# Kernel tuning notes

Measured on AMD Instinct MI355X. Metric: run time of the kernel, lower is better.

Reference implementation:

```python
import jax, jax.numpy as jnp
import numpy as np

N_NODES = 50000
N_EDGES = 1600000
GL = [512, 256, 16]
LL = [16, 16]


def setup_inputs() -> dict:
    key = jax.random.key(0)
    ks = jax.random.split(key, 10)
    H = jax.random.normal(ks[0], (N_NODES, GL[0]), dtype=jnp.float32)
    edge_index = jax.random.randint(ks[1], (2, N_EDGES), 0, N_NODES, dtype=jnp.int64)
    edge_vals = jax.random.uniform(ks[2], (N_EDGES,), dtype=jnp.float32)
    def uni(k, shape, fan_out):
        stdv = 1.0 / np.sqrt(fan_out)
        return jax.random.uniform(k, shape, minval=-stdv, maxval=stdv, dtype=jnp.float32)
    W1 = uni(ks[3], (GL[0], GL[1]), GL[1])
    b1 = uni(ks[4], (GL[1],), GL[1])
    W2 = uni(ks[5], (GL[1], GL[2]), GL[2])
    b2 = uni(ks[6], (GL[2],), GL[2])
    Wl = uni(ks[7], (LL[0], LL[1]), LL[0])
    bl = uni(ks[8], (LL[1],), LL[0])
    return {"H": H, "edge_index": edge_index, "edge_vals": edge_vals,
            "W1": W1, "b1": b1, "W2": W2, "b2": b2, "Wl": Wl, "bl": bl}


def reference(H, edge_index, edge_vals, W1, b1, W2, b2, Wl, bl):
    row, col = edge_index[0], edge_index[1]
    n = H.shape[0]

    def spmm(X):  # (A @ X) for sparse COO A, X: [N, d]
        return jax.ops.segment_sum(edge_vals[:, None] * X[col], row, num_segments=n)

    # graph conv layers (dropout condition idx < len-2 never fires with 2 layers)
    H1 = jax.nn.relu(spmm(H @ W1) + b1)
    H2 = jax.nn.relu(spmm(H1 @ W2) + b2)
    # linear head
    H3 = jax.nn.relu(H2 @ Wl + bl)
    Y = jax.nn.softmax(H3, axis=1)  # [N, g]

    # NCut loss: sum_e w_e * dot(Y[row_e]/Gamma, (1-Y)[col_e])
    D = jax.ops.segment_sum(edge_vals, row, num_segments=n)  # degree [N]
    Gamma = Y.T @ D  # [g]
    YbyG = Y / Gamma[None, :]
    loss = jnp.sum(jnp.sum(YbyG[row] * (1.0 - Y)[col], axis=1) * edge_vals)
    return jnp.reshape(loss, (1,))
```

## Files before the change

### kernel.cpp

```cpp
#include <hip/hip_runtime.h>


constexpr int NN = 50000;
constexpr int NE = 1600000;
constexpr int F0 = 512;
constexpr int F1 = 256;
constexpr int G  = 16;
constexpr int CB   = 196;
constexpr int CCAP = 10240;
constexpr int CHUNK = 4096;
constexpr int NGEMM = 391 * 2;
constexpr int NPASS = 391;

typedef short  s16x8 __attribute__((ext_vector_type(8)));
typedef float  f32x4 __attribute__((ext_vector_type(4)));
typedef float  f32x2 __attribute__((ext_vector_type(2)));
typedef int    i32x4 __attribute__((ext_vector_type(4)));
typedef int    i32x2 __attribute__((ext_vector_type(2)));
typedef float  fv4   __attribute__((ext_vector_type(4)));

static __device__ __forceinline__ unsigned short f2bf(float f) {
    union { float f; unsigned u; } v; v.f = f;
    unsigned r = (v.u + 0x7FFFu + ((v.u >> 16) & 1u)) >> 16;
    return (unsigned short)r;
}
static __device__ __forceinline__ float bf2f(unsigned short u) {
    union { unsigned u; float f; } v; v.u = (unsigned)u << 16;
    return v.f;
}

__global__ __launch_bounds__(256) void k_castW1(const float* __restrict__ W1, unsigned short* __restrict__ W1t) {
    int idx = blockIdx.x * 256 + threadIdx.x;
    if (idx < F0 * F1) {
        int k = idx >> 8, n = idx & 255;
        W1t[n * F0 + k] = f2bf(W1[idx]);
    }
}

__global__ __launch_bounds__(256) void k_fused1(const float* __restrict__ H,
                                                const unsigned short* __restrict__ W1t,
                                                unsigned char* __restrict__ XW,
                                                const int* __restrict__ row, const int* __restrict__ col,
                                                const float* __restrict__ ev,
                                                int* __restrict__ ccur, int2* __restrict__ cbuf) {
    __shared__ __align__(16) unsigned char smem[2 * 128 * 72 * 2];
    const int bid = blockIdx.x;
    const int tid = threadIdx.x;
    const int stripe = bid / 3;
    const int pos = bid - stripe * 3;

    if (pos != 1) {
        const int gidx = stripe * 2 + (pos >> 1);
        unsigned short (*As)[72] = (unsigned short(*)[72])smem;
        unsigned short (*Bs)[72] = (unsigned short(*)[72])(smem + 128 * 72 * 2);
        const int lane = tid & 63;
        const int wave = tid >> 6;
        const int bm = (gidx >> 1) * 128;
        const int bn = (gidx & 1) * 128;
        const int m_off = (wave & 1) * 64;
        const int n_off = (wave >> 1) * 64;
        const int l15  = lane & 15;
        const int quad = lane >> 4;

        f32x4 acc[4][4];
#pragma unroll
        for (int i = 0; i < 4; ++i)
#pragma unroll
            for (int j = 0; j < 4; ++j) acc[i][j] = (f32x4)0.f;

        const int arow = tid >> 4;
        const int akq  = tid & 15;
        const int brow = tid >> 3;
        const int bkq  = tid & 7;

        float4 ar[8];
        uint4  br[4];

#define LOAD_TILE(K0)                                                              \
        do {                                                                       \
            _Pragma("unroll")                                                      \
            for (int p = 0; p < 8; ++p) {                                          \
                int gr = bm + p * 16 + arow;                                       \
                ar[p] = (gr < NN)                                                  \
                    ? *(const float4*)&H[(size_t)gr * F0 + (K0) + akq * 4]         \
                    : make_float4(0.f, 0.f, 0.f, 0.f);                             \
            }                                                                      \
            _Pragma("unroll")                                                      \
            for (int p = 0; p < 4; ++p)                                            \
                br[p] = *(const uint4*)&W1t[(size_t)(bn + p * 32 + brow) * F0 + (K0) + bkq * 8]; \
        } while (0)

        LOAD_TILE(0);
        for (int k0 = 0; k0 < F0; k0 += 64) {
#pragma unroll
            for (int p = 0; p < 8; ++p) {
                unsigned d0 = (unsigned)f2bf(ar[p].x) | ((unsigned)f2bf(ar[p].y) << 16);
                unsigned d1 = (unsigned)f2bf(ar[p].z) | ((unsigned)f2bf(ar[p].w) << 16);
                *(uint2*)&As[p * 16 + arow][akq * 4] = make_uint2(d0, d1);
            }
#pragma unroll
            for (int p = 0; p < 4; ++p)
                *(uint4*)&Bs[p * 32 + brow][bkq * 8] = br[p];
            __syncthreads();
            if (k0 + 64 < F0) LOAD_TILE(k0 + 64);
#pragma unroll
            for (int kk = 0; kk < 64; kk += 32) {
                s16x8 af[4], bfr[4];
#pragma unroll
                for (int mi = 0; mi < 4; ++mi)
                    af[mi] = *(const s16x8*)&As[m_off + mi * 16 + l15][kk + quad * 8];
#pragma unroll
                for (int ni = 0; ni < 4; ++ni)
                    bfr[ni] = *(const s16x8*)&Bs[n_off + ni * 16 + l15][kk + quad * 8];
#pragma unroll
                for (int mi = 0; mi < 4; ++mi)
#pragma unroll
                    for (int ni = 0; ni < 4; ++ni)
                        acc[mi][ni] = __builtin_amdgcn_mfma_f32_16x16x32_bf16(af[mi], bfr[ni], acc[mi][ni], 0, 0, 0);
            }
            __syncthreads();
        }
#undef LOAD_TILE
#pragma unroll
        for (int mi = 0; mi < 4; ++mi) {
            int r0 = bm + m_off + mi * 16 + quad * 4;
#pragma unroll
            for (int reg = 0; reg < 4; ++reg) {
                int gr = r0 + reg;
                if (gr < NN) {
                    unsigned char* orow = &XW[(size_t)gr * F1 + bn + n_off];
#pragma unroll
                    for (int ni = 0; ni < 4; ++ni) {
                        int pk = __builtin_amdgcn_cvt_pk_fp8_f32(acc[mi][ni][reg], 0.f, 0, false);
                        orow[ni * 16 + l15] = (unsigned char)(pk & 0xff);
                    }
                }
            }
        }
    } else {
        int* hcnt  = (int*)smem;
        int* hbase = hcnt + CB;
        for (int i = tid; i < CB; i += 256) hcnt[i] = 0;
        __syncthreads();

        const int base4 = stripe * (CHUNK / 4);
        int recx[16]; float recw[16]; int cb[16];
#pragma unroll
        for (int k = 0; k < 4; ++k) {
            int i4 = base4 + k * 256 + tid;
            bool ok = i4 < NE / 4;
            i32x4 r = ok ? __builtin_nontemporal_load(&((const i32x4*)row)[i4]) : (i32x4)0;
            i32x4 c = ok ? __builtin_nontemporal_load(&((const i32x4*)col)[i4]) : (i32x4)0;
            fv4   w = ok ? __builtin_nontemporal_load(&((const fv4*)ev)[i4])   : (fv4)0.f;
            int rr[4] = {r.x, r.y, r.z, r.w};
            int cc[4] = {c.x, c.y, c.z, c.w};
            float ww[4] = {w.x, w.y, w.z, w.w};
#pragma unroll
            for (int j = 0; j < 4; ++j) {
                int slot = k * 4 + j;
                if (ok) {
                    cb[slot] = rr[j] >> 8;
                    atomicAdd(&hcnt[cb[slot]], 1);
                } else {
                    cb[slot] = -1;
                }
                recx[slot] = (cc[j] << 16) | (rr[j] & 255);
                recw[slot] = ww[j];
            }
        }
        __syncthreads();
        for (int i = tid; i < CB; i += 256) {
            int cnt = hcnt[i];
            hbase[i] = (cnt > 0) ? atomicAdd(&ccur[i], cnt) : 0;
            hcnt[i] = 0;
        }
        __syncthreads();
#pragma unroll
        for (int slot = 0; slot < 16; ++slot) {
            if (cb[slot] >= 0) {
                int p = hbase[cb[slot]] + atomicAdd(&hcnt[cb[slot]], 1);
                cbuf[(size_t)cb[slot] * CCAP + p] = make_int2(recx[slot], __float_as_int(recw[slot]));
            }
        }
    }
}

__global__ __launch_bounds__(256) void k_passB(const int2* __restrict__ cbuf, const int* __restrict__ ccur,
                                               int* __restrict__ rowptr, int2* __restrict__ E) {
    __shared__ int cnt[256];
    __shared__ int scn[256];
    __shared__ int red[4];
    const int cbk = blockIdx.x;
    const int tid = threadIdx.x;
    cnt[tid] = 0;

    int b = 0;
    for (int i = tid; i < cbk; i += 256) b += ccur[i];
#pragma unroll
    for (int off = 1; off < 64; off <<= 1) b += __shfl_xor(b, off, 64);
    if ((tid & 63) == 0) red[tid >> 6] = b;
    __syncthreads();
    const int base = red[0] + red[1] + red[2] + red[3];

    const int total = ccur[cbk];
    const int2* src = cbuf + (size_t)cbk * CCAP;
    for (int i = tid; i < total; i += 256) atomicAdd(&cnt[src[i].x & 255], 1);
    __syncthreads();

    scn[tid] = cnt[tid];
    __syncthreads();
    for (int off = 1; off < 256; off <<= 1) {
        int t = (tid >= off) ? scn[tid - off] : 0;
        __syncthreads();
        scn[tid] += t;
        __syncthreads();
    }
    const int excl = scn[tid] - cnt[tid];
    const int r = (cbk << 8) + tid;
    if (r <= NN) rowptr[r] = base + excl;
    __syncthreads();
    cnt[tid] = base + excl;
    __syncthreads();
    for (int i = tid; i < total; i += 256) {
        int2 rec = src[i];
        int rl = rec.x & 255;
        int c  = (int)((unsigned)rec.x >> 16);
        int p = atomicAdd(&cnt[rl], 1);
        E[p] = make_int2(c << 8, rec.y);
    }
}

__global__ __launch_bounds__(256) void k_spmm1(const unsigned char* __restrict__ XW, const int* __restrict__ rowptr,
                                               const int2* __restrict__ E,
                                               const float* __restrict__ b1, const float* __restrict__ W2,
                                               unsigned short* __restrict__ Z, float* __restrict__ Dv) {
    __shared__ float W2T[G * F1];
    const int tid = threadIdx.x;
#pragma unroll
    for (int it = 0; it < 16; ++it)
        W2T[it * 256 + tid] = W2[tid * 16 + it];
    __syncthreads();
    const int lane16 = tid & 15;
    const int loff = lane16 * 16;
    const int n = blockIdx.x * 16 + (tid >> 4);
    const int s = rowptr[n];
    const int e = rowptr[n + 1];
    const i32x2* Ev = (const i32x2*)E;

    float acc[16];
#pragma unroll
    for (int q = 0; q < 16; ++q) acc[q] = 0.f;
    float wsum = 0.f;

    for (int i = s; i < e; i += 4) {
        int of[4]; float w[4];
#pragma unroll
        for (int k = 0; k < 4; ++k) {
            int idx = i + k;
            bool ok = idx < e;
            i32x2 ed = __builtin_nontemporal_load(&Ev[ok ? idx : s]);
            of[k] = ed.x; w[k] = ok ? __int_as_float(ed.y) : 0.f;
        }
        uint4 gg[4];
#pragma unroll
        for (int k = 0; k < 4; ++k)
            gg[k] = *(const uint4*)(XW + of[k] + loff);
#pragma unroll
        for (int k = 0; k < 4; ++k) {
            const unsigned gw[4] = {gg[k].x, gg[k].y, gg[k].z, gg[k].w};
#pragma unroll
            for (int q = 0; q < 4; ++q) {
                f32x2 lo = __builtin_amdgcn_cvt_pk_f32_fp8(gw[q], false);
                f32x2 hi = __builtin_amdgcn_cvt_pk_f32_fp8(gw[q], true);
                acc[q * 4 + 0] = fmaf(w[k], lo.x, acc[q * 4 + 0]);
                acc[q * 4 + 1] = fmaf(w[k], lo.y, acc[q * 4 + 1]);
                acc[q * 4 + 2] = fmaf(w[k], hi.x, acc[q * 4 + 2]);
                acc[q * 4 + 3] = fmaf(w[k], hi.y, acc[q * 4 + 3]);
            }
            wsum += w[k];
        }
    }
    if (lane16 == 0) Dv[n] = wsum;

#pragma unroll
    for (int q = 0; q < 4; ++q) {
        float4 bb = *(const float4*)&b1[loff + q * 4];
        acc[q * 4 + 0] = fmaxf(acc[q * 4 + 0] + bb.x, 0.f);
        acc[q * 4 + 1] = fmaxf(acc[q * 4 + 1] + bb.y, 0.f);
        acc[q * 4 + 2] = fmaxf(acc[q * 4 + 2] + bb.z, 0.f);
        acc[q * 4 + 3] = fmaxf(acc[q * 4 + 3] + bb.w, 0.f);
    }

    float p[G];
#pragma unroll
    for (int j = 0; j < G; ++j) {
        float pj = 0.f;
#pragma unroll
        for (int q = 0; q < 4; ++q) {
            float4 w4 = *(const float4*)&W2T[j * F1 + loff + q * 4];
            pj += acc[q * 4 + 0] * w4.x + acc[q * 4 + 1] * w4.y
                + acc[q * 4 + 2] * w4.z + acc[q * 4 + 3] * w4.w;
        }
        p[j] = pj;
    }
#pragma unroll
    for (int off = 1; off < 16; off <<= 1) {
#pragma unroll
        for (int j = 0; j < G; ++j) p[j] += __shfl_xor(p[j], off, 64);
    }
    if (lane16 == 0) {
        unsigned zp[8];
#pragma unroll
        for (int j = 0; j < 8; ++j)
            zp[j] = (unsigned)f2bf(p[2 * j]) | ((unsigned)f2bf(p[2 * j + 1]) << 16);
        uint4* zo = (uint4*)&Z[n * G];
        zo[0] = make_uint4(zp[0], zp[1], zp[2], zp[3]);
        zo[1] = make_uint4(zp[4], zp[5], zp[6], zp[7]);
    }
}

__global__ __launch_bounds__(256) void k_head(const unsigned short* __restrict__ Zb, const int* __restrict__ rowptr,
                                              const int2* __restrict__ E,
                                              const float* __restrict__ b2, const float* __restrict__ Wl,
                                              const float* __restrict__ bl, const float* __restrict__ Dv,
                                              unsigned short* __restrict__ Yb, float* __restrict__ GammaP) {
    __shared__ float WlS[G * G];
    __shared__ float gsh[G];
    const int tid = threadIdx.x;
    if (tid < G * G) WlS[tid] = Wl[tid];
    if (tid < G) gsh[tid] = 0.f;
    __syncthreads();
    const int lane = tid & 63;
    const int g = lane >> 3;
    const int d = lane & 7;
    const int n = blockIdx.x * 4 + (tid >> 6);
    const int s = __builtin_amdgcn_readfirstlane(rowptr[n]);
    const int e = __builtin_amdgcn_readfirstlane(rowptr[n + 1]);
    const char* Zc = (const char*)Zb;
    const i32x2* Ev = (const i32x2*)E;

    float a0 = 0.f, a1 = 0.f;
    for (int base = s; base < e; base += 16) {
        int i0 = base + g;
        int i1 = base + 8 + g;
        i32x2 e0 = __builtin_nontemporal_load(&Ev[(i0 < e) ? i0 : s]);
        i32x2 e1 = __builtin_nontemporal_load(&Ev[(i1 < e) ? i1 : s]);
        float w0 = (i0 < e) ? __int_as_float(e0.y) : 0.f;
        float w1 = (i1 < e) ? __int_as_float(e1.y) : 0.f;
        unsigned z0 = *(const unsigned*)(Zc + (e0.x >> 3) + d * 4);
        unsigned z1 = *(const unsigned*)(Zc + (e1.x >> 3) + d * 4);
        a0 = fmaf(w0, bf2f((unsigned short)(z0 & 0xffff)), a0);
        a1 = fmaf(w0, bf2f((unsigned short)(z0 >> 16)), a1);
        a0 = fmaf(w1, bf2f((unsigned short)(z1 & 0xffff)), a0);
        a1 = fmaf(w1, bf2f((unsigned short)(z1 >> 16)), a1);
    }
    a0 += __shfl_xor(a0, 8, 64);  a1 += __shfl_xor(a1, 8, 64);
    a0 += __shfl_xor(a0, 16, 64); a1 += __shfl_xor(a1, 16, 64);
    a0 += __shfl_xor(a0, 32, 64); a1 += __shfl_xor(a1, 32, 64);

    const int j = lane & 15;
    float e0v = __shfl(a0, j >> 1, 64);
    float e1v = __shfl(a1, j >> 1, 64);
    float accj = (j & 1) ? e1v : e0v;

    float h2 = fmaxf(accj + b2[j], 0.f);
    float s3 = 0.f;
#pragma unroll
    for (int k = 0; k < G; ++k) s3 = fmaf(__shfl(h2, k, 64), WlS[k * G + j], s3);
    float h3 = fmaxf(s3 + bl[j], 0.f);
    float m = h3;
    m = fmaxf(m, __shfl_xor(m, 1, 64));
    m = fmaxf(m, __shfl_xor(m, 2, 64));
    m = fmaxf(m, __shfl_xor(m, 4, 64));
    m = fmaxf(m, __shfl_xor(m, 8, 64));
    float ex = __expf(h3 - m);
    float se = ex;
    se += __shfl_xor(se, 1, 64);
    se += __shfl_xor(se, 2, 64);
    se += __shfl_xor(se, 4, 64);
    se += __shfl_xor(se, 8, 64);
    float y = ex / se;
    if (lane < G) {
        Yb[n * G + j] = f2bf(y);
        atomicAdd(&gsh[j], y * Dv[n]);
    }
    __syncthreads();
    if (tid < G) atomicAdd(&GammaP[(blockIdx.x & 63) * G + tid], gsh[tid]);
}

__global__ __launch_bounds__(256) void k_loss(const unsigned short* __restrict__ Yb, const int* __restrict__ rowptr,
                                              const int2* __restrict__ E, float* __restrict__ SjP) {
    __shared__ float sjsh[G];
    const int tid = threadIdx.x;
    if (tid < G) sjsh[tid] = 0.f;
    __syncthreads();
    const int lane = tid & 63;
    const int g = lane >> 3;
    const int d = lane & 7;
    const int n = blockIdx.x * 4 + (tid >> 6);
    const int s = __builtin_amdgcn_readfirstlane(rowptr[n]);
    const int e = __builtin_amdgcn_readfirstlane(rowptr[n + 1]);
    const char* Yc = (const char*)Yb;
    const i32x2* Ev = (const i32x2*)E;

    unsigned yr = *(const unsigned*)(Yc + ((size_t)n << 5) + d * 4);
    float y0 = bf2f((unsigned short)(yr & 0xffff));
    float y1 = bf2f((unsigned short)(yr >> 16));

    float s0 = 0.f, s1 = 0.f;
    for (int base = s; base < e; base += 16) {
        int i0 = base + g;
        int i1 = base + 8 + g;
        i32x2 e0 = __builtin_nontemporal_load(&Ev[(i0 < e) ? i0 : s]);
        i32x2 e1 = __builtin_nontemporal_load(&Ev[(i1 < e) ? i1 : s]);
        float w0 = (i0 < e) ? __int_as_float(e0.y) : 0.f;
        float w1 = (i1 < e) ? __int_as_float(e1.y) : 0.f;
        unsigned z0 = *(const unsigned*)(Yc + (e0.x >> 3) + d * 4);
        unsigned z1 = *(const unsigned*)(Yc + (e1.x >> 3) + d * 4);
        s0 = fmaf(w0 * y0, bf2f((unsigned short)(z0 & 0xffff)), s0);
        s1 = fmaf(w0 * y1, bf2f((unsigned short)(z0 >> 16)), s1);
        s0 = fmaf(w1 * y0, bf2f((unsigned short)(z1 & 0xffff)), s0);
        s1 = fmaf(w1 * y1, bf2f((unsigned short)(z1 >> 16)), s1);
    }
    s0 += __shfl_xor(s0, 8, 64);  s1 += __shfl_xor(s1, 8, 64);
    s0 += __shfl_xor(s0, 16, 64); s1 += __shfl_xor(s1, 16, 64);
    s0 += __shfl_xor(s0, 32, 64); s1 += __shfl_xor(s1, 32, 64);
    if (lane < 8) {
        atomicAdd(&sjsh[2 * lane],     s0);
        atomicAdd(&sjsh[2 * lane + 1], s1);
    }
    __syncthreads();
    if (tid < G) atomicAdd(&SjP[(blockIdx.x & 63) * G + tid], sjsh[tid]);
}

__global__ void k_final(const float* __restrict__ GammaP, const float* __restrict__ SjP,
                        float* __restrict__ out) {
    const int tid = threadIdx.x;
    const int j = tid & 15;
    float gam = 0.f, sj = 0.f;
    for (int b = 0; b < 64; ++b) {
        gam += GammaP[b * G + j];
        sj  += SjP[b * G + j];
    }
    float v = sj / gam;
    v += __shfl_xor(v, 1, 64);
    v += __shfl_xor(v, 2, 64);
    v += __shfl_xor(v, 4, 64);
    v += __shfl_xor(v, 8, 64);
    if (tid == 0) out[0] = 16.0f - v;
}

static inline size_t alignup(size_t x) { return (x + 255) & ~(size_t)255; }

extern "C" void kernel_launch(void* const* d_in, const int* in_sizes, int n_in,
                              void* d_out, int out_size, void* d_ws, size_t ws_size,
                              hipStream_t stream) {
    const float* H  = (const float*)d_in[0];
    const int*   ei = (const int*)d_in[1];
    const float* ev = (const float*)d_in[2];
    const float* W1 = (const float*)d_in[3];
    const float* b1 = (const float*)d_in[4];
    const float* W2 = (const float*)d_in[5];
    const float* b2 = (const float*)d_in[6];
    const float* Wl = (const float*)d_in[7];
    const float* bl = (const float*)d_in[8];
    const int* row = ei;
    const int* col = ei + NE;

    char* base = (char*)d_ws;
    size_t off = 0;
    unsigned char*  XW  = (unsigned char*)(base + off);  off = alignup(off + (size_t)NN * F1);
    unsigned short* W1t = (unsigned short*)(base + off); off = alignup(off + (size_t)F0 * F1 * 2);
    unsigned short* Z   = (unsigned short*)(base + off); off = alignup(off + (size_t)NN * G * 2);
    unsigned short* Yb  = (unsigned short*)(base + off); off = alignup(off + (size_t)NN * G * 2);
    float* Dv     = (float*)(base + off); off = alignup(off + (size_t)NN * 4);
    size_t zoff = off;
    int*   ccur   = (int*)(base + off);   off += (size_t)CB * 4;
    float* GammaP = (float*)(base + off); off += (size_t)64 * G * 4;
    float* SjP    = (float*)(base + off); off += (size_t)64 * G * 4;
    size_t zsize = off - zoff;
    off = alignup(off);
    int*   rowptr = (int*)(base + off);   off = alignup(off + (size_t)(NN + 1) * 4);
    int2*  cbuf   = (int2*)(base + off);  off = alignup(off + (size_t)CB * CCAP * 8);
    int2*  E      = (int2*)(base + off);  off = alignup(off + (size_t)NE * 8);

    hipMemsetAsync(base + zoff, 0, zsize, stream);

    k_castW1<<<dim3((F0 * F1 + 255) / 256), dim3(256), 0, stream>>>(W1, W1t);
    k_fused1<<<dim3(3 * NPASS), dim3(256), 0, stream>>>(
        H, W1t, XW, row, col, ev, ccur, cbuf);
    k_passB<<<dim3(CB), dim3(256), 0, stream>>>(cbuf, ccur, rowptr, E);
    k_spmm1<<<dim3(NN / 16), dim3(256), 0, stream>>>(XW, rowptr, E, b1, W2, Z, Dv);
    k_head<<<dim3(NN / 4), dim3(256), 0, stream>>>(Z, rowptr, E, b2, Wl, bl, Dv, Yb, GammaP);
    k_loss<<<dim3(NN / 4), dim3(256), 0, stream>>>(Yb, rowptr, E, SjP);
    k_final<<<dim3(1), dim3(64), 0, stream>>>(GammaP, SjP, (float*)d_out);
}
```

Baseline: 397.5 us.

## Load GEMM tiles directly into LDS with swizzled layout, convert A to bf16 on read

Replaces the register-staged global loads in the fused H@W1 GEMM with global_load_lds direct-to-LDS transfers, keeping H in fp32 in LDS with an XOR swizzle. The bf16 packing moves to the fragment read using v_cvt_pk_bf16_f32. This is meant to cut VGPR pressure and the conversion and store instructions. In exchange the loop waits for each stage synchronously with no double buffering, so it loses the earlier overlap of loads with MFMA, and the fp32 A tile doubles LDS reads.

```diff
diff --git a/kernel.cpp b/kernel.cpp
--- a/kernel.cpp
+++ b/kernel.cpp
@@ -9,7 +9,6 @@
 constexpr int CB   = 196;
 constexpr int CCAP = 10240;
 constexpr int CHUNK = 4096;
-constexpr int NGEMM = 391 * 2;
 constexpr int NPASS = 391;
 
 typedef short  s16x8 __attribute__((ext_vector_type(8)));
@@ -29,6 +28,22 @@
     return v.f;
 }
 
+static __device__ __forceinline__ void glds16(const void* g, void* l) {
+    __builtin_amdgcn_global_load_lds(
+        (const __attribute__((address_space(1))) unsigned int*)g,
+        (__attribute__((address_space(3))) unsigned int*)l,
+        16, 0, 0);
+}
+
+static __device__ __forceinline__ s16x8 pack8(f32x4 a, f32x4 b) {
+    union { unsigned u[4]; s16x8 v; } r;
+    asm("v_cvt_pk_bf16_f32 %0, %1, %2" : "=v"(r.u[0]) : "v"(a.x), "v"(a.y));
+    asm("v_cvt_pk_bf16_f32 %0, %1, %2" : "=v"(r.u[1]) : "v"(a.z), "v"(a.w));
+    asm("v_cvt_pk_bf16_f32 %0, %1, %2" : "=v"(r.u[2]) : "v"(b.x), "v"(b.y));
+    asm("v_cvt_pk_bf16_f32 %0, %1, %2" : "=v"(r.u[3]) : "v"(b.z), "v"(b.w));
+    return r.v;
+}
+
 __global__ __launch_bounds__(256) void k_castW1(const float* __restrict__ W1, unsigned short* __restrict__ W1t) {
     int idx = blockIdx.x * 256 + threadIdx.x;
     if (idx < F0 * F1) {
@@ -43,7 +58,7 @@
                                                 const int* __restrict__ row, const int* __restrict__ col,
                                                 const float* __restrict__ ev,
                                                 int* __restrict__ ccur, int2* __restrict__ cbuf) {
-    __shared__ __align__(16) unsigned char smem[2 * 128 * 72 * 2];
+    __shared__ __align__(16) unsigned char smem[49152];
     const int bid = blockIdx.x;
     const int tid = threadIdx.x;
     const int stripe = bid / 3;
@@ -51,8 +66,6 @@
 
     if (pos != 1) {
         const int gidx = stripe * 2 + (pos >> 1);
-        unsigned short (*As)[72] = (unsigned short(*)[72])smem;
-        unsigned short (*Bs)[72] = (unsigned short(*)[72])(smem + 128 * 72 * 2);
         const int lane = tid & 63;
         const int wave = tid >> 6;
         const int bm = (gidx >> 1) * 128;
@@ -68,50 +81,52 @@
 #pragma unroll
             for (int j = 0; j < 4; ++j) acc[i][j] = (f32x4)0.f;
 
-        const int arow = tid >> 4;
-        const int akq  = tid & 15;
-        const int brow = tid >> 3;
-        const int bkq  = tid & 7;
-
-        float4 ar[8];
-        uint4  br[4];
-
-#define LOAD_TILE(K0)                                                              \
-        do {                                                                       \
-            _Pragma("unroll")                                                      \
-            for (int p = 0; p < 8; ++p) {                                          \
-                int gr = bm + p * 16 + arow;                                       \
-                ar[p] = (gr < NN)                                                  \
-                    ? *(const float4*)&H[(size_t)gr * F0 + (K0) + akq * 4]         \
-                    : make_float4(0.f, 0.f, 0.f, 0.f);                             \
-            }                                                                      \
-            _Pragma("unroll")                                                      \
-            for (int p = 0; p < 4; ++p)                                            \
-                br[p] = *(const uint4*)&W1t[(size_t)(bn + p * 32 + brow) * F0 + (K0) + bkq * 8]; \
+        const int arow16 = tid >> 4;
+        const int slA    = (tid & 15) ^ (arow16 & 7);
+        const int browB  = tid >> 3;
+        const int slB    = (tid & 7) ^ (browB & 7);
+        const int wvB    = wave * 1024;
+
+#define STAGE(K0)                                                              \
+        do {                                                                   \
+            _Pragma("unroll")                                                  \
+            for (int p = 0; p < 8; ++p) {                                      \
+                int gr = bm + p * 16 + arow16;                                 \
+                gr = gr < NN ? gr : NN - 1;                                    \
+                glds16(&H[(size_t)gr * F0 + (K0) + slA * 4],                   \
+                       smem + p * 4096 + wvB);                                 \
+            }                                                                  \
+            _Pragma("unroll")                                                  \
+            for (int p = 0; p < 4; ++p)                                        \
+                glds16(&W1t[(size_t)(bn + p * 32 + browB) * F0 + (K0) + slB * 8], \
+                       smem + 32768 + p * 4096 + wvB);                         \
         } while (0)
 
-        LOAD_TILE(0);
+        STAGE(0);
+        asm volatile("s_waitcnt vmcnt(0)" ::: "memory");
+        __syncthreads();
         for (int k0 = 0; k0 < F0; k0 += 64) {
 #pragma unroll
-            for (int p = 0; p < 8; ++p) {
-                unsigned d0 = (unsigned)f2bf(ar[p].x) | ((unsigned)f2bf(ar[p].y) << 16);
-                unsigned d1 = (unsigned)f2bf(ar[p].z) | ((unsigned)f2bf(ar[p].w) << 16);
-                *(uint2*)&As[p * 16 + arow][akq * 4] = make_uint2(d0, d1);
-            }
-#pragma unroll
-            for (int p = 0; p < 4; ++p)
-                *(uint4*)&Bs[p * 32 + brow][bkq * 8] = br[p];
-            __syncthreads();
-            if (k0 + 64 < F0) LOAD_TILE(k0 + 64);
-#pragma unroll
-            for (int kk = 0; kk < 64; kk += 32) {
+            for (int kk6 = 0; kk6 < 2; ++kk6) {
+                const int kk = kk6 * 32;
                 s16x8 af[4], bfr[4];
 #pragma unroll
-                for (int mi = 0; mi < 4; ++mi)
-                    af[mi] = *(const s16x8*)&As[m_off + mi * 16 + l15][kk + quad * 8];
-#pragma unroll
-                for (int ni = 0; ni < 4; ++ni)
-                    bfr[ni] = *(const s16x8*)&Bs[n_off + ni * 16 + l15][kk + quad * 8];
+                for (int mi = 0; mi < 4; ++mi) {
+                    const int r = m_off + mi * 16 + l15;
+                    const int sw = r & 7;
+                    const int s0 = (kk >> 2) + quad * 2;
+                    const char* rb = (const char*)smem + r * 256;
+                    f32x4 v0 = *(const f32x4*)(rb + (((s0    ) ^ sw) << 4));
+                    f32x4 v1 = *(const f32x4*)(rb + (((s0 + 1) ^ sw) << 4));
+                    af[mi] = pack8(v0, v1);
+                }
+#pragma unroll
+                for (int ni = 0; ni < 4; ++ni) {
+                    const int r = n_off + ni * 16 + l15;
+                    const int sb = (kk >> 3) + quad;
+                    bfr[ni] = *(const s16x8*)((const char*)smem + 32768 + r * 128
+                                              + ((sb ^ (r & 7)) << 4));
+                }
 #pragma unroll
                 for (int mi = 0; mi < 4; ++mi)
 #pragma unroll
@@ -119,8 +134,13 @@
                         acc[mi][ni] = __builtin_amdgcn_mfma_f32_16x16x32_bf16(af[mi], bfr[ni], acc[mi][ni], 0, 0, 0);
             }
             __syncthreads();
-        }
-#undef LOAD_TILE
+            if (k0 + 64 < F0) {
+                STAGE(k0 + 64);
+                asm volatile("s_waitcnt vmcnt(0)" ::: "memory");
+            }
+            __syncthreads();
+        }
+#undef STAGE
 #pragma unroll
         for (int mi = 0; mi < 4; ++mi) {
             int r0 = bm + m_off + mi * 16 + quad * 4;
```

After: 375.8 us. -5.5%, faster.
